# Kernel tuning notes

Measured on AMD Instinct MI355X. Metric: run time of the kernel, lower is better.

## Reference

```python
import jax, jax.numpy as jnp
import numpy as np

CAT_NUMS = 17   # cat_nums + 1 (background)
SCALE_NUMS = 5
DIM = 256
N = 1_000_000
T = 0.07        # InfoNCE temperature


def setup_inputs() -> dict:
    key = jax.random.key(0)
    k1, k2, k3, k4 = jax.random.split(key, 4)
    cls_feats = jax.random.normal(k1, (N, DIM), dtype=jnp.float32)
    cls_targets = jax.random.randint(k2, (N,), 0, CAT_NUMS)
    lvl_idx = jax.random.randint(k3, (N,), 0, SCALE_NUMS)
    prototypes = jax.random.normal(k4, (CAT_NUMS, SCALE_NUMS, DIM), dtype=jnp.float32) * 0.01
    return {"cls_feats": cls_feats, "cls_targets": cls_targets,
            "lvl_idx": lvl_idx, "prototypes": prototypes}


def reference(cls_feats, cls_targets, lvl_idx, prototypes):
    C, S, D = prototypes.shape
    n_seg = C * S
    # ---- update_mem_bank: fused segment-mean over (category, level) ----
    seg = cls_targets * S + lvl_idx                      # [N] combined segment id
    sums = jax.ops.segment_sum(cls_feats, seg, num_segments=n_seg)          # [C*S, D]
    counts = jax.ops.segment_sum(jnp.ones((cls_feats.shape[0],), cls_feats.dtype),
                                 seg, num_segments=n_seg)                   # [C*S]
    has = counts > 0                                      # mem_bank, [C*S]
    # empty segments keep the initial delta_prototype value of 0.01
    delta = jnp.where(has[:, None], sums / jnp.maximum(counts, 1.0)[:, None],
                      jnp.asarray(0.01, cls_feats.dtype)).reshape(C, S, D)
    delta = jax.lax.stop_gradient(delta)                  # torch .detach()
    mem_bank = has                                        # [C*S] in (cat, scale) order
    # ---- contrast_learning_update: InfoNCE(prototypes, delta) ----
    v1 = prototypes / jnp.linalg.norm(prototypes, axis=-1, keepdims=True)
    v2 = delta / jnp.linalg.norm(delta, axis=-1, keepdims=True)
    # bmm over scales: [S,C,D] x [S,D,C] -> [S,C,C] -> permute -> [C,S,C]
    logits = jnp.einsum('csd,ksd->csk', v1, v2) / T       # [C, S, C]
    logits = logits.reshape(-1, C)                        # [C*S, C]
    labels = jnp.tile(jnp.arange(C), S)                   # cat of arange(C), S times
    logp = jax.nn.log_softmax(logits, axis=-1)
    per_row = -logp[jnp.arange(C * S), labels]            # CE reduction='none'
    mask = mem_bank.astype(per_row.dtype)
    loss = jnp.sum(per_row * mask) / jnp.maximum(jnp.sum(mask), 1.0)
    return loss
```

## Files before the change

kernel.cpp:

```cpp
#include <hip/hip_runtime.h>
#include <hip/hip_bf16.h>

#define CATS 17
#define SCALES 5
#define DIM 256
#define NSEG (CATS * SCALES)
#define TEMP 0.07f
#define GPARTS 12
#define CHUNK_ROWS 4096

__global__ __launch_bounds__(256)
void build_kernel(const int* __restrict__ tgt, const int* __restrict__ lvl,
                  int* __restrict__ idx, int* __restrict__ gCnt,
                  int n, int idxStride) {
    __shared__ int hist[NSEG];
    __shared__ int baseb[NSEG];

    const int t  = threadIdx.x;
    const int r0 = blockIdx.x * CHUNK_ROWS;
    const int rbase = r0 + t * 16;

    for (int i = t; i < NSEG; i += 256) hist[i] = 0;
    __syncthreads();

    int segv[16];
    if (rbase + 16 <= n) {
        #pragma unroll
        for (int q = 0; q < 4; ++q) {
            const int4 tv = *reinterpret_cast<const int4*>(tgt + rbase + q * 4);
            const int4 lv = *reinterpret_cast<const int4*>(lvl + rbase + q * 4);
            segv[q * 4 + 0] = tv.x * SCALES + lv.x;
            segv[q * 4 + 1] = tv.y * SCALES + lv.y;
            segv[q * 4 + 2] = tv.z * SCALES + lv.z;
            segv[q * 4 + 3] = tv.w * SCALES + lv.w;
        }
    } else {
        #pragma unroll
        for (int k = 0; k < 16; ++k)
            segv[k] = (rbase + k < n)
                    ? tgt[rbase + k] * SCALES + lvl[rbase + k] : -1;
    }

    #pragma unroll
    for (int k = 0; k < 16; ++k)
        if (segv[k] >= 0) atomicAdd(&hist[segv[k]], 1);
    __syncthreads();

    for (int i = t; i < NSEG; i += 256)
        baseb[i] = atomicAdd(&gCnt[i], hist[i]);
    __syncthreads();
    for (int i = t; i < NSEG; i += 256) hist[i] = 0;
    __syncthreads();

    #pragma unroll
    for (int k = 0; k < 16; ++k) {
        const int s = segv[k];
        if (s >= 0) {
            const int rk = atomicAdd(&hist[s], 1);
            idx[(size_t)s * idxStride + baseb[s] + rk] = rbase + k;
        }
    }
}

__global__ __launch_bounds__(256)
void gather_kernel(const float* __restrict__ feats,
                   const int* __restrict__ idx,
                   const int* __restrict__ gCnt,
                   float* __restrict__ sums,
                   int idxStride) {
    const int bid  = blockIdx.x;
    const int g    = bid / GPARTS;
    const int p    = bid - g * GPARTS;
    const int lane = threadIdx.x & 63;
    const int wave = threadIdx.x >> 6;

    const int cnt   = gCnt[g];
    const int chunk = (cnt + GPARTS - 1) / GPARTS;
    const int e0    = p * chunk;
    const int e1    = min(e0 + chunk, cnt);
    const int* lst  = idx + (size_t)g * idxStride;

    float4 a0 = make_float4(0.f, 0.f, 0.f, 0.f), a1 = a0, a2 = a0, a3 = a0;
    float4 a4 = a0, a5 = a0, a6 = a0, a7 = a0;

    for (int e = e0 + wave * 64; e < e1; e += 256) {
        const int cntHere = min(64, e1 - e);
        const int ridv = lst[e + ((lane < cntHere) ? lane : 0)];

        if (cntHere == 64) {
            #pragma unroll
            for (int j0 = 0; j0 < 64; j0 += 8) {
                float4 v[8];
                #pragma unroll
                for (int u = 0; u < 8; ++u) {
                    const int sr = __shfl(ridv, j0 + u);
                    v[u] = *reinterpret_cast<const float4*>(
                        feats + (size_t)sr * DIM + lane * 4);
                }
                a0.x += v[0].x; a0.y += v[0].y; a0.z += v[0].z; a0.w += v[0].w;
                a1.x += v[1].x; a1.y += v[1].y; a1.z += v[1].z; a1.w += v[1].w;
                a2.x += v[2].x; a2.y += v[2].y; a2.z += v[2].z; a2.w += v[2].w;
                a3.x += v[3].x; a3.y += v[3].y; a3.z += v[3].z; a3.w += v[3].w;
                a4.x += v[4].x; a4.y += v[4].y; a4.z += v[4].z; a4.w += v[4].w;
                a5.x += v[5].x; a5.y += v[5].y; a5.z += v[5].z; a5.w += v[5].w;
                a6.x += v[6].x; a6.y += v[6].y; a6.z += v[6].z; a6.w += v[6].w;
                a7.x += v[7].x; a7.y += v[7].y; a7.z += v[7].z; a7.w += v[7].w;
            }
        } else {
            for (int j0 = 0; j0 < cntHere; j0 += 8) {
                float4 v[8]; float sc[8];
                #pragma unroll
                for (int u = 0; u < 8; ++u) {
                    const int jj = j0 + u;
                    const int jc = (jj < cntHere) ? jj : (cntHere - 1);
                    sc[u] = (jj < cntHere) ? 1.f : 0.f;
                    const int sr = __shfl(ridv, jc);
                    v[u] = *reinterpret_cast<const float4*>(
                        feats + (size_t)sr * DIM + lane * 4);
                }
                a0.x = fmaf(v[0].x, sc[0], a0.x); a0.y = fmaf(v[0].y, sc[0], a0.y);
                a0.z = fmaf(v[0].z, sc[0], a0.z); a0.w = fmaf(v[0].w, sc[0], a0.w);
                a1.x = fmaf(v[1].x, sc[1], a1.x); a1.y = fmaf(v[1].y, sc[1], a1.y);
                a1.z = fmaf(v[1].z, sc[1], a1.z); a1.w = fmaf(v[1].w, sc[1], a1.w);
                a2.x = fmaf(v[2].x, sc[2], a2.x); a2.y = fmaf(v[2].y, sc[2], a2.y);
                a2.z = fmaf(v[2].z, sc[2], a2.z); a2.w = fmaf(v[2].w, sc[2], a2.w);
                a3.x = fmaf(v[3].x, sc[3], a3.x); a3.y = fmaf(v[3].y, sc[3], a3.y);
                a3.z = fmaf(v[3].z, sc[3], a3.z); a3.w = fmaf(v[3].w, sc[3], a3.w);
                a4.x = fmaf(v[4].x, sc[4], a4.x); a4.y = fmaf(v[4].y, sc[4], a4.y);
                a4.z = fmaf(v[4].z, sc[4], a4.z); a4.w = fmaf(v[4].w, sc[4], a4.w);
                a5.x = fmaf(v[5].x, sc[5], a5.x); a5.y = fmaf(v[5].y, sc[5], a5.y);
                a5.z = fmaf(v[5].z, sc[5], a5.z); a5.w = fmaf(v[5].w, sc[5], a5.w);
                a6.x = fmaf(v[6].x, sc[6], a6.x); a6.y = fmaf(v[6].y, sc[6], a6.y);
                a6.z = fmaf(v[6].z, sc[6], a6.z); a6.w = fmaf(v[6].w, sc[6], a6.w);
                a7.x = fmaf(v[7].x, sc[7], a7.x); a7.y = fmaf(v[7].y, sc[7], a7.y);
                a7.z = fmaf(v[7].z, sc[7], a7.z); a7.w = fmaf(v[7].w, sc[7], a7.w);
            }
        }
    }

    a0.x += a1.x + a2.x + a3.x + a4.x + a5.x + a6.x + a7.x;
    a0.y += a1.y + a2.y + a3.y + a4.y + a5.y + a6.y + a7.y;
    a0.z += a1.z + a2.z + a3.z + a4.z + a5.z + a6.z + a7.z;
    a0.w += a1.w + a2.w + a3.w + a4.w + a5.w + a6.w + a7.w;

    float* dst = sums + (size_t)g * DIM + lane * 4;
    unsafeAtomicAdd(dst + 0, a0.x);
    unsafeAtomicAdd(dst + 1, a0.y);
    unsafeAtomicAdd(dst + 2, a0.z);
    unsafeAtomicAdd(dst + 3, a0.w);
}

__global__ void infonce_kernel(const float* __restrict__ protos,
                               const float* __restrict__ sums,
                               const int* __restrict__ gCnt,
                               float* __restrict__ numAcc) {
    const int cs   = blockIdx.x;
    const int s    = cs % SCALES;
    const int lane = threadIdx.x;

    const float4 p = *reinterpret_cast<const float4*>(
        protos + (size_t)cs * DIM + lane * 4);
    float ssq1 = p.x * p.x + p.y * p.y + p.z * p.z + p.w * p.w;
    #pragma unroll
    for (int off = 32; off > 0; off >>= 1) ssq1 += __shfl_down(ssq1, off);
    ssq1 = __shfl(ssq1, 0);

    float logits[CATS];
    for (int k = 0; k < CATS; ++k) {
        const int r2 = k * SCALES + s;
        const int cntv = gCnt[r2];
        float4 dv;
        if (cntv > 0) {
            const float4 sm = *reinterpret_cast<const float4*>(
                sums + (size_t)r2 * DIM + lane * 4);
            const float inv = 1.f / (float)cntv;
            dv = make_float4(sm.x * inv, sm.y * inv, sm.z * inv, sm.w * inv);
        } else {
            dv = make_float4(0.01f, 0.01f, 0.01f, 0.01f);
        }
        float ssq2 = dv.x * dv.x + dv.y * dv.y + dv.z * dv.z + dv.w * dv.w;
        float dot  = p.x * dv.x + p.y * dv.y + p.z * dv.z + p.w * dv.w;
        #pragma unroll
        for (int off = 32; off > 0; off >>= 1) {
            ssq2 += __shfl_down(ssq2, off);
            dot  += __shfl_down(dot, off);
        }
        const float lg = dot / (sqrtf(ssq2) * sqrtf(ssq1) * TEMP);
        logits[k] = __shfl(lg, 0);
    }

    if (lane == 0) {
        float m = logits[0];
        #pragma unroll
        for (int k = 1; k < CATS; ++k) m = fmaxf(m, logits[k]);
        float sum = 0.f;
        #pragma unroll
        for (int k = 0; k < CATS; ++k) sum += expf(logits[k] - m);
        const float lse     = m + logf(sum);
        const int   label   = cs % CATS;
        const float per_row = lse - logits[label];
        if (gCnt[cs] > 0) unsafeAtomicAdd(numAcc, per_row);
    }
}

__global__ void finalize_kernel(const int* __restrict__ gCnt,
                                const float* __restrict__ numAcc,
                                float* __restrict__ out) {
    float msum = 0.f;
    for (int i = 0; i < NSEG; ++i) msum += (gCnt[i] > 0) ? 1.f : 0.f;
    out[0] = numAcc[0] / fmaxf(msum, 1.f);
}

extern "C" void kernel_launch(void* const* d_in, const int* in_sizes, int n_in,
                              void* d_out, int out_size, void* d_ws, size_t ws_size,
                              hipStream_t stream) {
    const float* feats  = (const float*)d_in[0];
    const int*   tgt    = (const int*)d_in[1];
    const int*   lvl    = (const int*)d_in[2];
    const float* protos = (const float*)d_in[3];
    float* out = (float*)d_out;

    const int n = in_sizes[1];

    float* sums   = (float*)d_ws;
    float* numAcc = sums + NSEG * DIM;
    int*   gCnt   = (int*)(numAcc + 1);
    const size_t smallBytes = (size_t)(NSEG * DIM + 1 + NSEG) * 4;
    int* idx = (int*)((char*)d_ws + ((smallBytes + 127) & ~(size_t)127));

    hipMemsetAsync(d_ws, 0, smallBytes, stream);

    const int nBuild = (n + CHUNK_ROWS - 1) / CHUNK_ROWS;
    build_kernel<<<nBuild, 256, 0, stream>>>(tgt, lvl, idx, gCnt, n, n);
    gather_kernel<<<NSEG * GPARTS, 256, 0, stream>>>(feats, idx, gCnt, sums, n);
    infonce_kernel<<<NSEG, 64, 0, stream>>>(protos, sums, gCnt, numAcc);
    finalize_kernel<<<1, 1, 0, stream>>>(gCnt, numAcc, out);
}
```

Before: 218.7 us.

## Fold finalize into infonce, zero sums in build kernel, scalarize gather index loads

Removes the separate finalize launch: the last infonce block, detected with an atomic done-counter and thread fences, computes the masked mean and writes the output. The memset shrinks to the counters, and block 0 of the build kernel zeroes the sums buffer instead. In the gather kernel, row indices are read as wave-uniform loads through readfirstlane rather than broadcast with shuffles. This trims launch and memset overhead and per-row shuffles, at the cost of extra scalar loads and reliance on atomic ordering for the final reduction.

```diff
diff --git a/kernel.cpp b/kernel.cpp
--- a/kernel.cpp
+++ b/kernel.cpp
@@ -12,6 +12,7 @@
 __global__ __launch_bounds__(256)
 void build_kernel(const int* __restrict__ tgt, const int* __restrict__ lvl,
                   int* __restrict__ idx, int* __restrict__ gCnt,
+                  float* __restrict__ sums,
                   int n, int idxStride) {
     __shared__ int hist[NSEG];
     __shared__ int baseb[NSEG];
@@ -19,6 +20,12 @@
     const int t  = threadIdx.x;
     const int r0 = blockIdx.x * CHUNK_ROWS;
     const int rbase = r0 + t * 16;
+
+    if (blockIdx.x == 0) {
+        float4 z = make_float4(0.f, 0.f, 0.f, 0.f);
+        for (int i = t; i < NSEG * DIM / 4; i += 256)
+            reinterpret_cast<float4*>(sums)[i] = z;
+    }
 
     for (int i = t; i < NSEG; i += 256) hist[i] = 0;
     __syncthreads();
@@ -84,19 +91,20 @@
     float4 a4 = a0, a5 = a0, a6 = a0, a7 = a0;
 
     for (int e = e0 + wave * 64; e < e1; e += 256) {
-        const int cntHere = min(64, e1 - e);
-        const int ridv = lst[e + ((lane < cntHere) ? lane : 0)];
-
-        if (cntHere == 64) {
+        const int eu = __builtin_amdgcn_readfirstlane(e);
+        const int m  = min(64, e1 - eu);
+
+        if (m == 64) {
             #pragma unroll
             for (int j0 = 0; j0 < 64; j0 += 8) {
+                int id[8];
+                #pragma unroll
+                for (int u = 0; u < 8; ++u) id[u] = lst[eu + j0 + u];
                 float4 v[8];
                 #pragma unroll
-                for (int u = 0; u < 8; ++u) {
-                    const int sr = __shfl(ridv, j0 + u);
+                for (int u = 0; u < 8; ++u)
                     v[u] = *reinterpret_cast<const float4*>(
-                        feats + (size_t)sr * DIM + lane * 4);
-                }
+                        feats + (size_t)id[u] * DIM + lane * 4);
                 a0.x += v[0].x; a0.y += v[0].y; a0.z += v[0].z; a0.w += v[0].w;
                 a1.x += v[1].x; a1.y += v[1].y; a1.z += v[1].z; a1.w += v[1].w;
                 a2.x += v[2].x; a2.y += v[2].y; a2.z += v[2].z; a2.w += v[2].w;
@@ -107,17 +115,20 @@
                 a7.x += v[7].x; a7.y += v[7].y; a7.z += v[7].z; a7.w += v[7].w;
             }
         } else {
-            for (int j0 = 0; j0 < cntHere; j0 += 8) {
-                float4 v[8]; float sc[8];
+            for (int j0 = 0; j0 < m; j0 += 8) {
+                int id[8]; float sc[8];
                 #pragma unroll
                 for (int u = 0; u < 8; ++u) {
                     const int jj = j0 + u;
-                    const int jc = (jj < cntHere) ? jj : (cntHere - 1);
-                    sc[u] = (jj < cntHere) ? 1.f : 0.f;
-                    const int sr = __shfl(ridv, jc);
+                    const int jc = (jj < m) ? jj : (m - 1);
+                    sc[u] = (jj < m) ? 1.f : 0.f;
+                    id[u] = lst[eu + jc];
+                }
+                float4 v[8];
+                #pragma unroll
+                for (int u = 0; u < 8; ++u)
                     v[u] = *reinterpret_cast<const float4*>(
-                        feats + (size_t)sr * DIM + lane * 4);
-                }
+                        feats + (size_t)id[u] * DIM + lane * 4);
                 a0.x = fmaf(v[0].x, sc[0], a0.x); a0.y = fmaf(v[0].y, sc[0], a0.y);
                 a0.z = fmaf(v[0].z, sc[0], a0.z); a0.w = fmaf(v[0].w, sc[0], a0.w);
                 a1.x = fmaf(v[1].x, sc[1], a1.x); a1.y = fmaf(v[1].y, sc[1], a1.y);
@@ -153,7 +164,9 @@
 __global__ void infonce_kernel(const float* __restrict__ protos,
                                const float* __restrict__ sums,
                                const int* __restrict__ gCnt,
-                               float* __restrict__ numAcc) {
+                               float* __restrict__ numAcc,
+                               unsigned* __restrict__ doneCtr,
+                               float* __restrict__ out) {
     const int cs   = blockIdx.x;
     const int s    = cs % SCALES;
     const int lane = threadIdx.x;
@@ -190,25 +203,26 @@
     }
 
     if (lane == 0) {
-        float m = logits[0];
-        #pragma unroll
-        for (int k = 1; k < CATS; ++k) m = fmaxf(m, logits[k]);
+        float mx = logits[0];
+        #pragma unroll
+        for (int k = 1; k < CATS; ++k) mx = fmaxf(mx, logits[k]);
         float sum = 0.f;
         #pragma unroll
-        for (int k = 0; k < CATS; ++k) sum += expf(logits[k] - m);
-        const float lse     = m + logf(sum);
+        for (int k = 0; k < CATS; ++k) sum += expf(logits[k] - mx);
+        const float lse     = mx + logf(sum);
         const int   label   = cs % CATS;
         const float per_row = lse - logits[label];
-        if (gCnt[cs] > 0) unsafeAtomicAdd(numAcc, per_row);
-    }
-}
-
-__global__ void finalize_kernel(const int* __restrict__ gCnt,
-                                const float* __restrict__ numAcc,
-                                float* __restrict__ out) {
-    float msum = 0.f;
-    for (int i = 0; i < NSEG; ++i) msum += (gCnt[i] > 0) ? 1.f : 0.f;
-    out[0] = numAcc[0] / fmaxf(msum, 1.f);
+        unsafeAtomicAdd(numAcc, (gCnt[cs] > 0) ? per_row : 0.f);
+        __threadfence();
+        const unsigned done = atomicAdd(doneCtr, 1u);
+        if (done == NSEG - 1) {
+            __threadfence();
+            float msum = 0.f;
+            for (int i = 0; i < NSEG; ++i) msum += (gCnt[i] > 0) ? 1.f : 0.f;
+            const float total = unsafeAtomicAdd(numAcc, 0.f);
+            out[0] = total / fmaxf(msum, 1.f);
+        }
+    }
 }
 
 extern "C" void kernel_launch(void* const* d_in, const int* in_sizes, int n_in,
@@ -222,17 +236,17 @@
 
     const int n = in_sizes[1];
 
-    float* sums   = (float*)d_ws;
-    float* numAcc = sums + NSEG * DIM;
-    int*   gCnt   = (int*)(numAcc + 1);
-    const size_t smallBytes = (size_t)(NSEG * DIM + 1 + NSEG) * 4;
-    int* idx = (int*)((char*)d_ws + ((smallBytes + 127) & ~(size_t)127));
-
-    hipMemsetAsync(d_ws, 0, smallBytes, stream);
+    float*    numAcc  = (float*)d_ws;
+    unsigned* doneCtr = (unsigned*)((char*)d_ws + 4);
+    int*      gCnt    = (int*)((char*)d_ws + 8);
+    float*    sums    = (float*)((char*)d_ws + 512);
+    int*      idx     = (int*)((char*)d_ws + 512 + (size_t)NSEG * DIM * 4);
+
+    hipMemsetAsync(d_ws, 0, 8 + (size_t)NSEG * 4, stream);
 
     const int nBuild = (n + CHUNK_ROWS - 1) / CHUNK_ROWS;
-    build_kernel<<<nBuild, 256, 0, stream>>>(tgt, lvl, idx, gCnt, n, n);
+    build_kernel<<<nBuild, 256, 0, stream>>>(tgt, lvl, idx, gCnt, sums, n, n);
     gather_kernel<<<NSEG * GPARTS, 256, 0, stream>>>(feats, idx, gCnt, sums, n);
-    infonce_kernel<<<NSEG, 64, 0, stream>>>(protos, sums, gCnt, numAcc);
-    finalize_kernel<<<1, 1, 0, stream>>>(gCnt, numAcc, out);
-}
+    infonce_kernel<<<NSEG, 64, 0, stream>>>(protos, sums, gCnt, numAcc,
+                                            doneCtr, out);
+}
```

Result: slower. 225.4 us (+3.1%).
